# Kernel tuning notes

Hardware: AMD Instinct MI355X
Metric: run time of the kernel (lower is better)

## Reference

```python
import jax, jax.numpy as jnp
import numpy as np

N = 100000
E = 3200000
H_MLP = 30   # EdgeMLP hidden dim
H_GCN = 10   # GCNEvaluator hidden dim
D_IN = 6     # node_dim + token_dim


def setup_inputs() -> dict:
    key = jax.random.key(0)
    ks = jax.random.split(key, 24)
    s = 0.1
    inp = {
        "x": jax.random.normal(ks[0], (N, 1), jnp.float32),
        "token": jax.random.normal(ks[1], (N, 5), jnp.float32),
        "edge_attr_gen": jax.random.normal(ks[2], (E, 1), jnp.float32),
        "edge_attr_eval": jax.random.uniform(ks[3], (E, 2), jnp.float32),
        "gumbel": jax.random.gumbel(ks[4], (E, 2), jnp.float32),
        "edge_index": jax.random.randint(ks[5], (2, E), 0, N, jnp.int32),
        # EdgeMLP params: Linear(13,30), Linear(30,30), Linear(30,30), Linear(30,2)
        "W0": jax.random.normal(ks[6], (2 * D_IN + 1, H_MLP), jnp.float32) * s,
        "b0": jnp.zeros((H_MLP,), jnp.float32),
        "W1": jax.random.normal(ks[7], (H_MLP, H_MLP), jnp.float32) * s,
        "b1": jnp.zeros((H_MLP,), jnp.float32),
        "W2": jax.random.normal(ks[8], (H_MLP, H_MLP), jnp.float32) * s,
        "b2": jnp.zeros((H_MLP,), jnp.float32),
        "W3": jax.random.normal(ks[9], (H_MLP, 2), jnp.float32) * s,
        "b3": jnp.zeros((2,), jnp.float32),
        # GCNEvaluator params
        "Wl": jax.random.normal(ks[10], (1, 1), jnp.float32) * s,   # edge_weight_lin
        "bl": jnp.zeros((1,), jnp.float32),
        "Wc": jax.random.normal(ks[11], (D_IN, H_GCN), jnp.float32) * s,  # GCNConv weight
        "bc": jnp.zeros((H_GCN,), jnp.float32),
        "Wo": jax.random.normal(ks[12], (H_GCN, 1), jnp.float32) * s,     # output Linear
        "bo": jnp.zeros((1,), jnp.float32),
    }
    return inp


def reference(x, token, edge_attr_gen, edge_attr_eval, gumbel, edge_index,
              W0, b0, W1, b1, W2, b2, W3, b3, Wl, bl, Wc, bc, Wo, bo):
    src = edge_index[0]
    tgt = edge_index[1]
    x_all = jnp.concatenate([x, token], axis=-1)              # [N, 6]

    # ---- generate_graph: edge gather + concat + MLP ----
    ef = jnp.concatenate([x_all[src], x_all[tgt], edge_attr_gen], axis=-1)  # [E, 13]
    h = jax.nn.relu(ef @ W0 + b0)
    h = jax.nn.relu(h @ W1 + b1)
    h = jax.nn.relu(h @ W2 + b2)
    logits = h @ W3 + b3                                      # [E, 2]

    # gumbel_softmax(tau=1.0, hard=True) with straight-through
    y_soft = jax.nn.softmax(logits + gumbel, axis=-1)
    y_hard = jax.nn.one_hot(jnp.argmax(y_soft, axis=-1), 2, dtype=y_soft.dtype)
    y = y_hard + y_soft - jax.lax.stop_gradient(y_soft)
    edge_value = y[:, 1:2]                                    # [E, 1]

    # ---- evaluate_graph: GCNEvaluator ----
    combined = jnp.concatenate([edge_attr_eval, edge_value], axis=-1)  # [E, 3]
    mask = combined[:, -2] * (1.0 - combined[:, -1])
    ew = jax.nn.sigmoid((combined[:, :1] @ Wl + bl)[:, 0]) * mask      # [E]

    # GCNConv(add_self_loops=True, normalize=True)
    loop = jnp.arange(N, dtype=src.dtype)
    row = jnp.concatenate([src, loop])
    col = jnp.concatenate([tgt, loop])
    w = jnp.concatenate([ew, jnp.ones((N,), ew.dtype)])
    deg = jax.ops.segment_sum(w, col, num_segments=N)
    dis = jnp.where(deg > 0, jax.lax.rsqrt(jnp.where(deg > 0, deg, 1.0)), 0.0)
    norm = dis[row] * w * dis[col]
    xw = x_all @ Wc                                            # [N, 10]
    agg = jax.ops.segment_sum(norm[:, None] * xw[row], col, num_segments=N) + bc
    out = jax.nn.sigmoid(agg @ Wo + bo)                        # [N, 1]
    return out
```

## Files before the change

### kernel.cpp

```cpp
#include <hip/hip_runtime.h>

#define NN 100000
#define NE 3200000
#define HM 30
#define HG 10
#define MAXK 26
#define OVF_CAP 8192

typedef float __attribute__((ext_vector_type(2))) f32x2;

__device__ __forceinline__ f32x2 pkfma(f32x2 a, f32x2 b, f32x2 c) {
#if __has_builtin(__builtin_elementwise_fma)
    return __builtin_elementwise_fma(a, b, c);
#else
    f32x2 r; r.x = fmaf(a.x, b.x, c.x); r.y = fmaf(a.y, b.y, c.y); return r;
#endif
}

__global__ __launch_bounds__(256) void wtrans_kernel(
    const float* __restrict__ W0, const float* __restrict__ W1,
    const float* __restrict__ W2,
    float* __restrict__ W0T, float* __restrict__ W1T, float* __restrict__ W2T)
{
    for (int idx = threadIdx.x; idx < HM * 16; idx += 256) {
        int j = idx >> 4, i = idx & 15;
        W0T[idx] = (i < 13) ? W0[i * HM + j] : 0.f;
    }
    for (int idx = threadIdx.x; idx < HM * 32; idx += 256) {
        int j = idx >> 5, i = idx & 31;
        float v1 = (i < HM) ? W1[i * HM + j] : 0.f;
        float v2 = (i < HM) ? W2[i * HM + j] : 0.f;
        W1T[idx] = v1;
        W2T[idx] = v2;
    }
}

__global__ __launch_bounds__(256) void pack_kernel(
    const float* __restrict__ x, const float* __restrict__ token,
    const float* __restrict__ Wc,
    float* __restrict__ xall8, float* __restrict__ xwp)
{
    __shared__ float sWc[6 * HG];
    if (threadIdx.x < 6 * HG) sWc[threadIdx.x] = Wc[threadIdx.x];
    __syncthreads();

    int n = blockIdx.x * 256 + threadIdx.x;
    if (n >= NN) return;

    float xa[6];
    xa[0] = x[n];
    #pragma unroll
    for (int i = 0; i < 5; i++) xa[1 + i] = token[n * 5 + i];

    float4* x4 = (float4*)xall8;
    x4[n * 2 + 0] = make_float4(xa[0], xa[1], xa[2], xa[3]);
    x4[n * 2 + 1] = make_float4(xa[4], xa[5], 0.f, 0.f);

    float w[12];
    #pragma unroll
    for (int k = 0; k < HG; k++) {
        float a = 0.f;
        #pragma unroll
        for (int i = 0; i < 6; i++) a = fmaf(xa[i], sWc[i * HG + k], a);
        w[k] = a;
    }
    w[10] = 0.f; w[11] = 0.f;
    float4* wp = (float4*)(xwp + (size_t)n * 12);
    wp[0] = make_float4(w[0], w[1], w[2], w[3]);
    wp[1] = make_float4(w[4], w[5], w[6], w[7]);
    wp[2] = make_float4(w[8], w[9], w[10], w[11]);
}

__global__ __launch_bounds__(256, 2) void edge_mlp7_kernel(
    const float* __restrict__ xall8,
    const float* __restrict__ eg, const float* __restrict__ ee,
    const float* __restrict__ gum, const int* __restrict__ eidx,
    const float* __restrict__ W0T, const float* __restrict__ b0,
    const float* __restrict__ W1T, const float* __restrict__ b1,
    const float* __restrict__ W2T, const float* __restrict__ b2,
    const float* __restrict__ W3, const float* __restrict__ b3,
    const float* __restrict__ Wl, const float* __restrict__ bl,
    float2* __restrict__ slots, int* __restrict__ cnt,
    int* __restrict__ ohead, int* __restrict__ onxt,
    float* __restrict__ ovf_w, int* __restrict__ ovf_s, int* __restrict__ novf)
{
    int e = blockIdx.x * 256 + threadIdx.x;
    int s = eidx[e];
    int t = eidx[NE + e];

    const float4* x4 = (const float4*)xall8;
    float4 qa = x4[s * 2], qb = x4[s * 2 + 1];
    float4 qc = x4[t * 2], qd = x4[t * 2 + 1];

    f32x2 ef2[7];
    ef2[0] = f32x2{ qa.x, qa.y };
    ef2[1] = f32x2{ qa.z, qa.w };
    ef2[2] = f32x2{ qb.x, qb.y };
    ef2[3] = f32x2{ qc.x, qc.y };
    ef2[4] = f32x2{ qc.z, qc.w };
    ef2[5] = f32x2{ qd.x, qd.y };
    ef2[6] = f32x2{ eg[e], 0.f };

    float h[HM], g[HM];

    #pragma unroll
    for (int j = 0; j < HM; j++) {
        const f32x2* w2 = (const f32x2*)(W0T + j * 16);
        f32x2 a2 = f32x2{ b0[j], 0.f };
        #pragma unroll
        for (int p = 0; p < 7; p++) a2 = pkfma(ef2[p], w2[p], a2);
        h[j] = fmaxf(a2.x + a2.y, 0.f);
    }

    {
        f32x2 hp[15];
        #pragma unroll
        for (int p = 0; p < 15; p++) hp[p] = f32x2{ h[2 * p], h[2 * p + 1] };
        #pragma unroll
        for (int j = 0; j < HM; j++) {
            const f32x2* w2 = (const f32x2*)(W1T + j * 32);
            f32x2 a2 = f32x2{ b1[j], 0.f };
            #pragma unroll
            for (int p = 0; p < 15; p++) a2 = pkfma(hp[p], w2[p], a2);
            g[j] = fmaxf(a2.x + a2.y, 0.f);
        }
    }
    {
        f32x2 gp[15];
        #pragma unroll
        for (int p = 0; p < 15; p++) gp[p] = f32x2{ g[2 * p], g[2 * p + 1] };
        #pragma unroll
        for (int j = 0; j < HM; j++) {
            const f32x2* w2 = (const f32x2*)(W2T + j * 32);
            f32x2 a2 = f32x2{ b2[j], 0.f };
            #pragma unroll
            for (int p = 0; p < 15; p++) a2 = pkfma(gp[p], w2[p], a2);
            h[j] = fmaxf(a2.x + a2.y, 0.f);
        }
    }

    float l0 = b3[0], l1 = b3[1];
    #pragma unroll
    for (int i = 0; i < HM; i++) {
        l0 = fmaf(h[i], W3[i * 2 + 0], l0);
        l1 = fmaf(h[i], W3[i * 2 + 1], l1);
    }

    const float2 g2 = ((const float2*)gum)[e];
    float v0 = l0 + g2.x;
    float v1 = l1 + g2.y;

    float ew = 0.f;
    if (!(v1 > v0)) {
        const float2 e2 = ((const float2*)ee)[e];
        float z = fmaf(e2.x, Wl[0], bl[0]);
        ew = e2.y / (1.f + __expf(-z));
    }
    if (ew != 0.f) {
        int slot = atomicAdd(&cnt[t], 1);
        if (slot < MAXK) {
            slots[(size_t)t * MAXK + slot] = make_float2(ew, __int_as_float(s));
        } else {
            int i = atomicAdd(novf, 1);
            if (i < OVF_CAP) {
                ovf_w[i] = ew;
                ovf_s[i] = s;
                onxt[i] = atomicExch(&ohead[t], i);
            }
        }
    }
}

__global__ __launch_bounds__(256) void node_deg_kernel(
    const float2* __restrict__ slots, const int* __restrict__ cnt,
    const int* __restrict__ ohead, const int* __restrict__ onxt,
    const float* __restrict__ ovf_w,
    float* __restrict__ xwp, float* __restrict__ dis)
{
    int n = blockIdx.x * 256 + threadIdx.x;
    if (n >= NN) return;

    int c = cnt[n];
    int cc = c < MAXK ? c : MAXK;
    float deg = 0.f;
    for (int j = 0; j < cc; j++) deg += slots[(size_t)n * MAXK + j].x;
    for (int i = ohead[n]; i >= 0; i = onxt[i]) deg += ovf_w[i];

    float d = rsqrtf(deg + 1.0f);
    dis[n] = d;

    float4* wp = (float4*)(xwp + (size_t)n * 12);
    #pragma unroll
    for (int q = 0; q < 3; q++) {
        float4 v = wp[q];
        v.x *= d; v.y *= d; v.z *= d; v.w *= d;
        wp[q] = v;
    }
}

__global__ __launch_bounds__(256) void gather_out5_kernel(
    const float2* __restrict__ slots, const int* __restrict__ cnt,
    const int* __restrict__ ohead, const int* __restrict__ onxt,
    const float* __restrict__ ovf_w, const int* __restrict__ ovf_s,
    const float* __restrict__ z, const float* __restrict__ dis,
    const float* __restrict__ bc, const float* __restrict__ Wo,
    const float* __restrict__ bo, float* __restrict__ out)
{
    __shared__ float sbc[12], sWo[12], sbo;
    if (threadIdx.x < 12) {
        sbc[threadIdx.x] = (threadIdx.x < HG) ? bc[threadIdx.x] : 0.f;
        sWo[threadIdx.x] = (threadIdx.x < HG) ? Wo[threadIdx.x] : 0.f;
    }
    if (threadIdx.x == 0) sbo = bo[0];
    __syncthreads();

    int tg = blockIdx.x * 256 + threadIdx.x;
    int n = tg >> 3;
    int k = tg & 7;
    if (n >= NN) return;

    const float4* Z = (const float4*)z;
    float4 A0 = make_float4(0.f, 0.f, 0.f, 0.f), A1 = A0, A2 = A0;

    int c = cnt[n];
    int cc = c < MAXK ? c : MAXK;
    for (int j = k; j < cc; j += 8) {
        float2 p = slots[(size_t)n * MAXK + j];
        float w = p.x;
        int s = __float_as_int(p.y);
        float4 z0 = Z[s * 3], z1 = Z[s * 3 + 1], z2 = Z[s * 3 + 2];
        A0.x = fmaf(w, z0.x, A0.x); A0.y = fmaf(w, z0.y, A0.y);
        A0.z = fmaf(w, z0.z, A0.z); A0.w = fmaf(w, z0.w, A0.w);
        A1.x = fmaf(w, z1.x, A1.x); A1.y = fmaf(w, z1.y, A1.y);
        A1.z = fmaf(w, z1.z, A1.z); A1.w = fmaf(w, z1.w, A1.w);
        A2.x = fmaf(w, z2.x, A2.x); A2.y = fmaf(w, z2.y, A2.y);
    }
    if (k == 0) {
        for (int i = ohead[n]; i >= 0; i = onxt[i]) {
            float w = ovf_w[i];
            int s = ovf_s[i];
            float4 z0 = Z[s * 3], z1 = Z[s * 3 + 1], z2 = Z[s * 3 + 2];
            A0.x = fmaf(w, z0.x, A0.x); A0.y = fmaf(w, z0.y, A0.y);
            A0.z = fmaf(w, z0.z, A0.z); A0.w = fmaf(w, z0.w, A0.w);
            A1.x = fmaf(w, z1.x, A1.x); A1.y = fmaf(w, z1.y, A1.y);
            A1.z = fmaf(w, z1.z, A1.z); A1.w = fmaf(w, z1.w, A1.w);
            A2.x = fmaf(w, z2.x, A2.x); A2.y = fmaf(w, z2.y, A2.y);
        }
        float4 s0 = Z[n * 3], s1 = Z[n * 3 + 1], s2 = Z[n * 3 + 2];
        A0.x += s0.x; A0.y += s0.y; A0.z += s0.z; A0.w += s0.w;
        A1.x += s1.x; A1.y += s1.y; A1.z += s1.z; A1.w += s1.w;
        A2.x += s2.x; A2.y += s2.y;
    }

    float v[10] = { A0.x, A0.y, A0.z, A0.w, A1.x, A1.y, A1.z, A1.w, A2.x, A2.y };
    #pragma unroll
    for (int q = 0; q < 10; q++) {
        v[q] += __shfl_xor(v[q], 1);
        v[q] += __shfl_xor(v[q], 2);
        v[q] += __shfl_xor(v[q], 4);
    }

    if (k == 0) {
        float d = dis[n];
        float o = sbo;
        #pragma unroll
        for (int q = 0; q < HG; q++)
            o = fmaf(fmaf(v[q], d, sbc[q]), sWo[q], o);
        out[n] = 1.f / (1.f + __expf(-o));
    }
}

__global__ __launch_bounds__(256) void edge_mlp_kernel(
    const float* __restrict__ x, const float* __restrict__ token,
    const float* __restrict__ eg, const float* __restrict__ ee,
    const float* __restrict__ gum, const int* __restrict__ eidx,
    const float* __restrict__ W0, const float* __restrict__ b0,
    const float* __restrict__ W1, const float* __restrict__ b1,
    const float* __restrict__ W2, const float* __restrict__ b2,
    const float* __restrict__ W3, const float* __restrict__ b3,
    const float* __restrict__ Wl, const float* __restrict__ bl,
    float* __restrict__ ew_out, float* __restrict__ deg)
{
    __shared__ float sW0[13 * HM];
    __shared__ float sW1[HM * HM];
    __shared__ float sW2[HM * HM];
    __shared__ float sW3f[HM * 2];
    __shared__ float sb0[HM], sb1[HM], sb2[HM], sb3[2];
    __shared__ float sWl, sbl;

    for (int i = threadIdx.x; i < 13 * HM; i += 256) sW0[i] = W0[i];
    for (int i = threadIdx.x; i < HM * HM; i += 256) sW1[i] = W1[i];
    for (int i = threadIdx.x; i < HM * HM; i += 256) sW2[i] = W2[i];
    for (int i = threadIdx.x; i < HM * 2; i += 256) sW3f[i] = W3[i];
    if (threadIdx.x < HM) {
        sb0[threadIdx.x] = b0[threadIdx.x];
        sb1[threadIdx.x] = b1[threadIdx.x];
        sb2[threadIdx.x] = b2[threadIdx.x];
    }
    if (threadIdx.x < 2) sb3[threadIdx.x] = b3[threadIdx.x];
    if (threadIdx.x == 0) { sWl = Wl[0]; sbl = bl[0]; }
    __syncthreads();

    int e = blockIdx.x * 256 + threadIdx.x;
    if (e >= NE) return;
    int s = eidx[e];
    int t = eidx[NE + e];

    float ef[13];
    ef[0] = x[s];
    #pragma unroll
    for (int i = 0; i < 5; i++) ef[1 + i] = token[s * 5 + i];
    ef[6] = x[t];
    #pragma unroll
    for (int i = 0; i < 5; i++) ef[7 + i] = token[t * 5 + i];
    ef[12] = eg[e];

    float h[HM], h2[HM];
    #pragma unroll
    for (int j = 0; j < HM; j++) {
        float a = sb0[j];
        #pragma unroll
        for (int i = 0; i < 13; i++) a = fmaf(ef[i], sW0[i * HM + j], a);
        h[j] = a > 0.f ? a : 0.f;
    }
    #pragma unroll
    for (int j = 0; j < HM; j++) {
        float a = sb1[j];
        #pragma unroll
        for (int i = 0; i < HM; i++) a = fmaf(h[i], sW1[i * HM + j], a);
        h2[j] = a > 0.f ? a : 0.f;
    }
    #pragma unroll
    for (int j = 0; j < HM; j++) {
        float a = sb2[j];
        #pragma unroll
        for (int i = 0; i < HM; i++) a = fmaf(h2[i], sW2[i * HM + j], a);
        h[j] = a > 0.f ? a : 0.f;
    }
    float l0 = sb3[0], l1 = sb3[1];
    #pragma unroll
    for (int i = 0; i < HM; i++) {
        l0 = fmaf(h[i], sW3f[i * 2 + 0], l0);
        l1 = fmaf(h[i], sW3f[i * 2 + 1], l1);
    }
    const float2 g2 = ((const float2*)gum)[e];
    float v0 = l0 + g2.x, v1 = l1 + g2.y;
    float ew = 0.f;
    if (!(v1 > v0)) {
        const float2 ee2 = ((const float2*)ee)[e];
        float z = fmaf(ee2.x, sWl, sbl);
        ew = ee2.y / (1.f + __expf(-z));
    }
    ew_out[e] = ew;
    if (ew != 0.f) atomicAdd(&deg[t], ew);
}

__global__ __launch_bounds__(256) void node_pre_kernel(
    const float* __restrict__ x, const float* __restrict__ token,
    const float* __restrict__ Wc, const float* __restrict__ deg,
    float* __restrict__ xw, float* __restrict__ dis)
{
    __shared__ float sWc[6 * HG];
    if (threadIdx.x < 6 * HG) sWc[threadIdx.x] = Wc[threadIdx.x];
    __syncthreads();
    int n = blockIdx.x * 256 + threadIdx.x;
    if (n >= NN) return;
    float xa[6];
    xa[0] = x[n];
    #pragma unroll
    for (int i = 0; i < 5; i++) xa[1 + i] = token[n * 5 + i];
    #pragma unroll
    for (int k = 0; k < HG; k++) {
        float a = 0.f;
        #pragma unroll
        for (int i = 0; i < 6; i++) a = fmaf(xa[i], sWc[i * HG + k], a);
        xw[n * HG + k] = a;
    }
    dis[n] = rsqrtf(deg[n] + 1.0f);
}

__global__ __launch_bounds__(256) void edge_scatter_kernel(
    const int* __restrict__ eidx, const float* __restrict__ ew,
    const float* __restrict__ dis, const float* __restrict__ xw,
    float* __restrict__ agg)
{
    int e = blockIdx.x * 256 + threadIdx.x;
    if (e >= NE) return;
    float w = ew[e];
    if (w == 0.f) return;
    int s = eidx[e];
    int t = eidx[NE + e];
    float norm = dis[s] * w * dis[t];
    #pragma unroll
    for (int k = 0; k < HG; k++)
        atomicAdd(&agg[t * HG + k], norm * xw[s * HG + k]);
}

__global__ __launch_bounds__(256) void node_out_kernel(
    const float* __restrict__ agg, const float* __restrict__ xw,
    const float* __restrict__ dis, const float* __restrict__ bc,
    const float* __restrict__ Wo, const float* __restrict__ bo,
    float* __restrict__ out)
{
    __shared__ float sbc[HG], sWo[HG], sbo;
    if (threadIdx.x < HG) { sbc[threadIdx.x] = bc[threadIdx.x]; sWo[threadIdx.x] = Wo[threadIdx.x]; }
    if (threadIdx.x == 0) sbo = bo[0];
    __syncthreads();
    int n = blockIdx.x * 256 + threadIdx.x;
    if (n >= NN) return;
    float d = dis[n];
    float self = d * d;
    float acc = sbo;
    #pragma unroll
    for (int k = 0; k < HG; k++) {
        float v = agg[n * HG + k] + xw[n * HG + k] * self + sbc[k];
        acc = fmaf(v, sWo[k], acc);
    }
    out[n] = 1.f / (1.f + __expf(-acc));
}

extern "C" void kernel_launch(void* const* d_in, const int* in_sizes, int n_in,
                              void* d_out, int out_size, void* d_ws, size_t ws_size,
                              hipStream_t stream) {
    const float* x   = (const float*)d_in[0];
    const float* tok = (const float*)d_in[1];
    const float* eg  = (const float*)d_in[2];
    const float* ee  = (const float*)d_in[3];
    const float* gum = (const float*)d_in[4];
    const int*   ei  = (const int*)d_in[5];
    const float* W0  = (const float*)d_in[6];
    const float* b0  = (const float*)d_in[7];
    const float* W1  = (const float*)d_in[8];
    const float* b1  = (const float*)d_in[9];
    const float* W2  = (const float*)d_in[10];
    const float* b2  = (const float*)d_in[11];
    const float* W3  = (const float*)d_in[12];
    const float* b3  = (const float*)d_in[13];
    const float* Wl  = (const float*)d_in[14];
    const float* bl  = (const float*)d_in[15];
    const float* Wc  = (const float*)d_in[16];
    const float* bc  = (const float*)d_in[17];
    const float* Wo  = (const float*)d_in[18];
    const float* bo  = (const float*)d_in[19];
    float* out = (float*)d_out;

    dim3 blk(256);
    dim3 egrid(NE / 256);
    dim3 ngrid((NN + 255) / 256);
    dim3 g8grid((NN * 8 + 255) / 256);

    size_t off_xall8 = 0;
    size_t off_xwp   = off_xall8 + (size_t)NN * 8;
    size_t off_slots = off_xwp + (size_t)NN * 12;
    size_t off_cnt   = off_slots + (size_t)NN * MAXK * 2;
    size_t off_novf  = off_cnt + NN;
    size_t off_dis   = off_novf + 1;
    size_t off_ohead = off_dis + NN;
    size_t off_ovfw  = off_ohead + NN;
    size_t off_ovfs  = off_ovfw + OVF_CAP;
    size_t off_onxt  = off_ovfs + OVF_CAP;
    size_t off_w0t   = (off_onxt + OVF_CAP + 15) & ~(size_t)15;
    size_t off_w1t   = off_w0t + 30 * 16;
    size_t off_w2t   = off_w1t + 30 * 32;
    size_t need_new  = (off_w2t + 30 * 32) * sizeof(float);

    if (ws_size >= need_new) {
        float*  ws    = (float*)d_ws;
        float*  xall8 = ws + off_xall8;
        float*  xwp   = ws + off_xwp;
        float2* slots = (float2*)(ws + off_slots);
        int*    cnt   = (int*)(ws + off_cnt);
        int*    novf  = (int*)(ws + off_novf);
        float*  dis   = ws + off_dis;
        int*    ohead = (int*)(ws + off_ohead);
        float*  ovf_w = ws + off_ovfw;
        int*    ovf_s = (int*)(ws + off_ovfs);
        int*    onxt  = (int*)(ws + off_onxt);
        float*  W0T   = ws + off_w0t;
        float*  W1T   = ws + off_w1t;
        float*  W2T   = ws + off_w2t;

        hipMemsetAsync(cnt, 0, (size_t)(NN + 1) * sizeof(int), stream);
        hipMemsetAsync(ohead, 0xFF, (size_t)NN * sizeof(int), stream);

        wtrans_kernel<<<dim3(1), blk, 0, stream>>>(W0, W1, W2, W0T, W1T, W2T);
        pack_kernel<<<ngrid, blk, 0, stream>>>(x, tok, Wc, xall8, xwp);
        edge_mlp7_kernel<<<egrid, blk, 0, stream>>>(xall8, eg, ee, gum, ei,
                                                    W0T, b0, W1T, b1, W2T, b2,
                                                    W3, b3, Wl, bl, slots, cnt,
                                                    ohead, onxt, ovf_w, ovf_s, novf);
        node_deg_kernel<<<ngrid, blk, 0, stream>>>(slots, cnt, ohead, onxt, ovf_w,
                                                   xwp, dis);
        gather_out5_kernel<<<g8grid, blk, 0, stream>>>(slots, cnt, ohead, onxt,
                                                       ovf_w, ovf_s, xwp, dis,
                                                       bc, Wo, bo, out);
    } else {
        float* ws  = (float*)d_ws;
        float* ew  = ws;
        float* deg = ew + NE;
        float* agg = deg + NN;
        float* xw  = agg + (size_t)NN * HG;
        float* dis = xw + (size_t)NN * HG;

        hipMemsetAsync(deg, 0, (size_t)(NN + (size_t)NN * HG) * sizeof(float), stream);
        edge_mlp_kernel<<<egrid, blk, 0, stream>>>(x, tok, eg, ee, gum, ei,
                                                   W0, b0, W1, b1, W2, b2, W3, b3,
                                                   Wl, bl, ew, deg);
        node_pre_kernel<<<ngrid, blk, 0, stream>>>(x, tok, Wc, deg, xw, dis);
        edge_scatter_kernel<<<egrid, blk, 0, stream>>>(ei, ew, dis, xw, agg);
        node_out_kernel<<<ngrid, blk, 0, stream>>>(agg, xw, dis, bc, Wo, bo, out);
    }
}
```

Baseline: 372.2 us.

## Pad node feature rows to 64 bytes and split degree reduction across 4 lanes

The per-node transformed feature rows (xw scaled by dis) are padded from 48 to 64 bytes when workspace allows, so each random source-row gather in the aggregation kernel touches a single aligned 64-byte segment instead of straddling cache lines. The degree kernel now uses 4 threads per node, each summing a strided subset of slots, combines them with shuffles, and lets each lane rescale one float4 of the row. The cost is more workspace and more memory footprint for the padded rows, plus extra shuffle and launch-width overhead in the degree kernel.

```diff
diff --git a/kernel.cpp b/kernel.cpp
--- a/kernel.cpp
+++ b/kernel.cpp
@@ -38,7 +38,7 @@
 __global__ __launch_bounds__(256) void pack_kernel(
     const float* __restrict__ x, const float* __restrict__ token,
     const float* __restrict__ Wc,
-    float* __restrict__ xall8, float* __restrict__ xwp)
+    float* __restrict__ xall8, float* __restrict__ xwp, int zr)
 {
     __shared__ float sWc[6 * HG];
     if (threadIdx.x < 6 * HG) sWc[threadIdx.x] = Wc[threadIdx.x];
@@ -65,7 +65,7 @@
         w[k] = a;
     }
     w[10] = 0.f; w[11] = 0.f;
-    float4* wp = (float4*)(xwp + (size_t)n * 12);
+    float4* wp = (float4*)xwp + (size_t)n * zr;
     wp[0] = make_float4(w[0], w[1], w[2], w[3]);
     wp[1] = make_float4(w[4], w[5], w[6], w[7]);
     wp[2] = make_float4(w[8], w[9], w[10], w[11]);
@@ -171,30 +171,35 @@
     }
 }
 
-__global__ __launch_bounds__(256) void node_deg_kernel(
+__global__ __launch_bounds__(256) void node_deg4_kernel(
     const float2* __restrict__ slots, const int* __restrict__ cnt,
     const int* __restrict__ ohead, const int* __restrict__ onxt,
     const float* __restrict__ ovf_w,
-    float* __restrict__ xwp, float* __restrict__ dis)
-{
-    int n = blockIdx.x * 256 + threadIdx.x;
+    float* __restrict__ xwp, float* __restrict__ dis, int zr)
+{
+    int tg = blockIdx.x * 256 + threadIdx.x;
+    int n = tg >> 2;
+    int k = tg & 3;
     if (n >= NN) return;
 
     int c = cnt[n];
     int cc = c < MAXK ? c : MAXK;
     float deg = 0.f;
-    for (int j = 0; j < cc; j++) deg += slots[(size_t)n * MAXK + j].x;
-    for (int i = ohead[n]; i >= 0; i = onxt[i]) deg += ovf_w[i];
+    for (int j = k; j < cc; j += 4) deg += slots[(size_t)n * MAXK + j].x;
+    if (k == 0)
+        for (int i = ohead[n]; i >= 0; i = onxt[i]) deg += ovf_w[i];
+
+    deg += __shfl_xor(deg, 1);
+    deg += __shfl_xor(deg, 2);
 
     float d = rsqrtf(deg + 1.0f);
-    dis[n] = d;
-
-    float4* wp = (float4*)(xwp + (size_t)n * 12);
-    #pragma unroll
-    for (int q = 0; q < 3; q++) {
-        float4 v = wp[q];
+    if (k == 0) dis[n] = d;
+
+    if (k < 3) {
+        float4* wp = (float4*)xwp + (size_t)n * zr;
+        float4 v = wp[k];
         v.x *= d; v.y *= d; v.z *= d; v.w *= d;
-        wp[q] = v;
+        wp[k] = v;
     }
 }
 
@@ -204,7 +209,7 @@
     const float* __restrict__ ovf_w, const int* __restrict__ ovf_s,
     const float* __restrict__ z, const float* __restrict__ dis,
     const float* __restrict__ bc, const float* __restrict__ Wo,
-    const float* __restrict__ bo, float* __restrict__ out)
+    const float* __restrict__ bo, float* __restrict__ out, int zr)
 {
     __shared__ float sbc[12], sWo[12], sbo;
     if (threadIdx.x < 12) {
@@ -228,7 +233,8 @@
         float2 p = slots[(size_t)n * MAXK + j];
         float w = p.x;
         int s = __float_as_int(p.y);
-        float4 z0 = Z[s * 3], z1 = Z[s * 3 + 1], z2 = Z[s * 3 + 2];
+        size_t row = (size_t)s * zr;
+        float4 z0 = Z[row], z1 = Z[row + 1], z2 = Z[row + 2];
         A0.x = fmaf(w, z0.x, A0.x); A0.y = fmaf(w, z0.y, A0.y);
         A0.z = fmaf(w, z0.z, A0.z); A0.w = fmaf(w, z0.w, A0.w);
         A1.x = fmaf(w, z1.x, A1.x); A1.y = fmaf(w, z1.y, A1.y);
@@ -239,14 +245,16 @@
         for (int i = ohead[n]; i >= 0; i = onxt[i]) {
             float w = ovf_w[i];
             int s = ovf_s[i];
-            float4 z0 = Z[s * 3], z1 = Z[s * 3 + 1], z2 = Z[s * 3 + 2];
+            size_t row = (size_t)s * zr;
+            float4 z0 = Z[row], z1 = Z[row + 1], z2 = Z[row + 2];
             A0.x = fmaf(w, z0.x, A0.x); A0.y = fmaf(w, z0.y, A0.y);
             A0.z = fmaf(w, z0.z, A0.z); A0.w = fmaf(w, z0.w, A0.w);
             A1.x = fmaf(w, z1.x, A1.x); A1.y = fmaf(w, z1.y, A1.y);
             A1.z = fmaf(w, z1.z, A1.z); A1.w = fmaf(w, z1.w, A1.w);
             A2.x = fmaf(w, z2.x, A2.x); A2.y = fmaf(w, z2.y, A2.y);
         }
-        float4 s0 = Z[n * 3], s1 = Z[n * 3 + 1], s2 = Z[n * 3 + 2];
+        size_t row = (size_t)n * zr;
+        float4 s0 = Z[row], s1 = Z[row + 1], s2 = Z[row + 2];
         A0.x += s0.x; A0.y += s0.y; A0.z += s0.z; A0.w += s0.w;
         A1.x += s1.x; A1.y += s1.y; A1.z += s1.z; A1.w += s1.w;
         A2.x += s2.x; A2.y += s2.y;
@@ -447,53 +455,67 @@
     dim3 blk(256);
     dim3 egrid(NE / 256);
     dim3 ngrid((NN + 255) / 256);
+    dim3 n4grid((NN * 4 + 255) / 256);
     dim3 g8grid((NN * 8 + 255) / 256);
 
-    size_t off_xall8 = 0;
-    size_t off_xwp   = off_xall8 + (size_t)NN * 8;
-    size_t off_slots = off_xwp + (size_t)NN * 12;
-    size_t off_cnt   = off_slots + (size_t)NN * MAXK * 2;
-    size_t off_novf  = off_cnt + NN;
-    size_t off_dis   = off_novf + 1;
-    size_t off_ohead = off_dis + NN;
-    size_t off_ovfw  = off_ohead + NN;
-    size_t off_ovfs  = off_ovfw + OVF_CAP;
-    size_t off_onxt  = off_ovfs + OVF_CAP;
-    size_t off_w0t   = (off_onxt + OVF_CAP + 15) & ~(size_t)15;
-    size_t off_w1t   = off_w0t + 30 * 16;
-    size_t off_w2t   = off_w1t + 30 * 32;
-    size_t need_new  = (off_w2t + 30 * 32) * sizeof(float);
-
-    if (ws_size >= need_new) {
+    auto compute_need = [&](size_t zs, size_t* offs) {
+        size_t off_xall8 = 0;
+        size_t off_xwp   = off_xall8 + (size_t)NN * 8;
+        size_t off_slots = off_xwp + (size_t)NN * zs;
+        size_t off_cnt   = off_slots + (size_t)NN * MAXK * 2;
+        size_t off_novf  = off_cnt + NN;
+        size_t off_dis   = off_novf + 1;
+        size_t off_ohead = off_dis + NN;
+        size_t off_ovfw  = off_ohead + NN;
+        size_t off_ovfs  = off_ovfw + OVF_CAP;
+        size_t off_onxt  = off_ovfs + OVF_CAP;
+        size_t off_w0t   = (off_onxt + OVF_CAP + 15) & ~(size_t)15;
+        size_t off_w1t   = off_w0t + 30 * 16;
+        size_t off_w2t   = off_w1t + 30 * 32;
+        offs[0] = off_xall8; offs[1] = off_xwp; offs[2] = off_slots;
+        offs[3] = off_cnt;   offs[4] = off_novf; offs[5] = off_dis;
+        offs[6] = off_ohead; offs[7] = off_ovfw; offs[8] = off_ovfs;
+        offs[9] = off_onxt;  offs[10] = off_w0t; offs[11] = off_w1t;
+        offs[12] = off_w2t;
+        return (off_w2t + 30 * 32) * sizeof(float);
+    };
+
+    size_t offs[13];
+    size_t zs = 16;
+    size_t need = compute_need(zs, offs);
+    if (ws_size < need) { zs = 12; need = compute_need(zs, offs); }
+
+    if (ws_size >= need) {
+        int zr = (int)(zs / 4);
         float*  ws    = (float*)d_ws;
-        float*  xall8 = ws + off_xall8;
-        float*  xwp   = ws + off_xwp;
-        float2* slots = (float2*)(ws + off_slots);
-        int*    cnt   = (int*)(ws + off_cnt);
-        int*    novf  = (int*)(ws + off_novf);
-        float*  dis   = ws + off_dis;
-        int*    ohead = (int*)(ws + off_ohead);
-        float*  ovf_w = ws + off_ovfw;
-        int*    ovf_s = (int*)(ws + off_ovfs);
-        int*    onxt  = (int*)(ws + off_onxt);
-        float*  W0T   = ws + off_w0t;
-        float*  W1T   = ws + off_w1t;
-        float*  W2T   = ws + off_w2t;
+        float*  xall8 = ws + offs[0];
+        float*  xwp   = ws + offs[1];
+        float2* slots = (float2*)(ws + offs[2]);
+        int*    cnt   = (int*)(ws + offs[3]);
+        int*    novf  = (int*)(ws + offs[4]);
+        float*  dis   = ws + offs[5];
+        int*    ohead = (int*)(ws + offs[6]);
+        float*  ovf_w = ws + offs[7];
+        int*    ovf_s = (int*)(ws + offs[8]);
+        int*    onxt  = (int*)(ws + offs[9]);
+        float*  W0T   = ws + offs[10];
+        float*  W1T   = ws + offs[11];
+        float*  W2T   = ws + offs[12];
 
         hipMemsetAsync(cnt, 0, (size_t)(NN + 1) * sizeof(int), stream);
         hipMemsetAsync(ohead, 0xFF, (size_t)NN * sizeof(int), stream);
 
         wtrans_kernel<<<dim3(1), blk, 0, stream>>>(W0, W1, W2, W0T, W1T, W2T);
-        pack_kernel<<<ngrid, blk, 0, stream>>>(x, tok, Wc, xall8, xwp);
+        pack_kernel<<<ngrid, blk, 0, stream>>>(x, tok, Wc, xall8, xwp, zr);
         edge_mlp7_kernel<<<egrid, blk, 0, stream>>>(xall8, eg, ee, gum, ei,
                                                     W0T, b0, W1T, b1, W2T, b2,
                                                     W3, b3, Wl, bl, slots, cnt,
                                                     ohead, onxt, ovf_w, ovf_s, novf);
-        node_deg_kernel<<<ngrid, blk, 0, stream>>>(slots, cnt, ohead, onxt, ovf_w,
-                                                   xwp, dis);
+        node_deg4_kernel<<<n4grid, blk, 0, stream>>>(slots, cnt, ohead, onxt,
+                                                     ovf_w, xwp, dis, zr);
         gather_out5_kernel<<<g8grid, blk, 0, stream>>>(slots, cnt, ohead, onxt,
                                                        ovf_w, ovf_s, xwp, dis,
-                                                       bc, Wo, bo, out);
+                                                       bc, Wo, bo, out, zr);
     } else {
         float* ws  = (float*)d_ws;
         float* ew  = ws;
```

Result: no change. 371.0 us (-0.3%).
